# Performance work log

Measured on AMD Instinct MI355X. Metric: run time of the kernel, lower is better.

Reference implementation:

```python
import jax, jax.numpy as jnp
import numpy as np

T = 0.05  # temperature
Z = 8     # number of nearest neighbours


def setup_inputs() -> dict:
    key = jax.random.key(0)
    k1, k2 = jax.random.split(key)
    prototypes = jax.random.normal(k1, (2048, 128), dtype=jnp.float32)
    prototypes = prototypes / jnp.linalg.norm(prototypes, axis=-1, keepdims=True)
    memory_points = jax.random.normal(k2, (131072, 128), dtype=jnp.float32)
    memory_points = memory_points / jnp.linalg.norm(memory_points, axis=-1, keepdims=True)
    return {"prototypes": prototypes, "memory_points": memory_points}


def reference(prototypes, memory_points):
    # [P, N] similarity, exp-scaled (monotonic, kept for faithfulness to the torch code)
    sim = jnp.exp(jnp.einsum('pd,nd->pn', prototypes, memory_points) / T)
    # top-z neighbours per prototype (largest, sorted) -> indices [P, Z]
    _, idx = jax.lax.top_k(sim, Z)
    # gather neighbour points [P, Z, D] and average over the Z neighbours
    pseudo_pro = memory_points[idx].sum(axis=1) / Z  # [P, D]
    # MSELoss with default 'mean' reduction
    loss = jnp.mean((pseudo_pro - prototypes) ** 2)
    return loss
```

## Files before the change

### kernel.cpp

```cpp
#include <hip/hip_runtime.h>
#include <float.h>

#define P 2048
#define N 131072
#define D 128
#define GP 32
#define PBG (P / (GP * 4))
#define NSW 128
#define NPW (N / NSW)
#define NT32 (NPW / 32)
#define CAP 192
#define LCAP 768
#define QS 192.0f
#define VEFF_I 10580
#define VEFF 0.286f

typedef short bf16x8 __attribute__((ext_vector_type(8)));
typedef float f32x4  __attribute__((ext_vector_type(4)));
typedef int   i32x4  __attribute__((ext_vector_type(4)));

union B128 { uint4 u; bf16x8 h; };
union U4I  { uint4 u; i32x4 i; };

__device__ __forceinline__ unsigned int f2bf(float f) {
  unsigned int u = __float_as_uint(f);
  return (u + 0x7FFFu + ((u >> 16) & 1u)) >> 16;
}

__device__ __forceinline__ uint4 pack8(float a0, float a1, float a2, float a3,
                                       float a4, float a5, float a6, float a7) {
  uint4 o;
  o.x = f2bf(a0) | (f2bf(a1) << 16);
  o.y = f2bf(a2) | (f2bf(a3) << 16);
  o.z = f2bf(a4) | (f2bf(a5) << 16);
  o.w = f2bf(a6) | (f2bf(a7) << 16);
  return o;
}

__device__ __forceinline__ unsigned q8(float x) {
  int v = (int)rintf(x * QS);
  v = min(127, max(-127, v));
  return (unsigned)(v & 0xFF);
}

__device__ __forceinline__ unsigned q8x4(const float* r) {
  return q8(r[0]) | (q8(r[1]) << 8) | (q8(r[2]) << 16) | (q8(r[3]) << 24);
}

__device__ __forceinline__ void gld_lds16(const uint4* g, uint4* l) {
  __builtin_amdgcn_global_load_lds((const __attribute__((address_space(1))) void*)g,
                                   (__attribute__((address_space(3))) void*)l, 16, 0, 0);
}

__global__ __launch_bounds__(256) void pack_i8_kernel(
    const float* __restrict__ protos, const float* __restrict__ mem,
    uint4* __restrict__ pPack, uint4* __restrict__ mPack,
    int* __restrict__ cnt, float* __restrict__ out)
{
  __shared__ float lds[32][132];

  const int bi  = blockIdx.x;
  const int tid = threadIdx.x;
  if (bi < 8) { cnt[bi * 256 + tid] = 0; if (bi == 0 && tid == 0) out[0] = 0.0f; }

  const float* src; uint4* dst; int r32;
  if (bi < 64) { src = protos; dst = pPack; r32 = bi; }
  else         { src = mem;    dst = mPack; r32 = bi - 64; }

  #pragma unroll
  for (int i = 0; i < 4; ++i) {
    const int idx = i * 256 + tid;
    const int rr  = idx >> 5;
    const int j   = idx & 31;
    const float4 v = *(const float4*)(src + ((size_t)r32 * 32 + rr) * D + j * 4);
    *(float4*)&lds[rr][j * 4] = v;
  }
  __syncthreads();

  const int h    = tid >> 7;
  const int kt   = (tid >> 6) & 1;
  const int lane = tid & 63;
  const int rowl = h * 16 + (lane & 15);
  const int lw   = lane >> 4;
  const int d0   = kt * 64 + lw * 16;
  const float* r = &lds[rowl][d0];
  uint4 o;
  o.x = q8x4(r);
  o.y = q8x4(r + 4);
  o.z = q8x4(r + 8);
  o.w = q8x4(r + 12);
  dst[(size_t)r32 * 256 + tid] = o;
}

__global__ __launch_bounds__(256, 8) void filter_kernel(
    const uint4* __restrict__ pPack, const uint4* __restrict__ mPack,
    int* __restrict__ cnt, int* __restrict__ cand)
{
  __shared__ uint4 sB[4][256];
  __shared__ unsigned lbuf[LCAP];
  __shared__ int lcnt;

  const int lane = threadIdx.x & 63;
  const int wq   = threadIdx.x >> 6;
  const int b    = blockIdx.x;
  const int xcd  = b & 7;
  const int t8   = b >> 3;
  const int ns   = xcd * (NSW / 8) + (t8 >> 4);
  const int pg   = (t8 & 15) * 4 + wq;
  const int lr   = lane & 15;
  const int lw   = lane >> 4;
  const int prb  = pg * GP + (lw << 2);

  i32x4 A0[2], A1[2];
  #pragma unroll
  for (int kt = 0; kt < 2; ++kt) {
    U4I t0, t1;
    t0.u = pPack[(size_t)((pg * 2 + 0) * 128 + kt * 64) + lane];
    t1.u = pPack[(size_t)((pg * 2 + 1) * 128 + kt * 64) + lane];
    A0[kt] = t0.i;
    A1[kt] = t1.i;
  }

  if (threadIdx.x == 0) lcnt = 0;

#define STAGE(tt, bb)                                                          \
  do {                                                                         \
    const uint4* gsrc = mPack + (size_t)(ns * NT32 + (tt)) * 256;              \
    gld_lds16(gsrc + wq * 64 + lane, &sB[bb][wq * 64]);                        \
  } while (0)

#define APPEND(CV, ROFF)                                                       \
  _Pragma("unroll")                                                            \
  for (int j = 0; j < 4; ++j) {                                                \
    if (CV[j] > VEFF_I) {                                                      \
      const int pr = prb + (ROFF) + j;                                         \
      const int s  = atomicAdd(&lcnt, 1);                                      \
      if (s < LCAP) {                                                          \
        lbuf[s] = ((unsigned)pr << 17) | (unsigned)ptb;                        \
      } else {                                                                 \
        const int gs = atomicAdd(&cnt[pr], 1);                                 \
        if (gs < CAP) cand[(size_t)pr * CAP + gs] = ptb;                       \
      }                                                                        \
    }                                                                          \
  }

#define TILE_BODY(TT)                                                          \
  do {                                                                         \
    const uint4* buf = &sB[(TT) & 3][0];                                       \
    _Pragma("unroll")                                                          \
    for (int h = 0; h < 2; ++h) {                                              \
      U4I b0, b1;                                                              \
      b0.u = buf[h * 128 + 0 * 64 + lane];                                     \
      b1.u = buf[h * 128 + 1 * 64 + lane];                                     \
      i32x4 c0 = {0, 0, 0, 0}, c1 = {0, 0, 0, 0};                              \
      c0 = __builtin_amdgcn_mfma_i32_16x16x64_i8(A0[0], b0.i, c0, 0, 0, 0);    \
      c1 = __builtin_amdgcn_mfma_i32_16x16x64_i8(A1[0], b0.i, c1, 0, 0, 0);    \
      c0 = __builtin_amdgcn_mfma_i32_16x16x64_i8(A0[1], b1.i, c0, 0, 0, 0);    \
      c1 = __builtin_amdgcn_mfma_i32_16x16x64_i8(A1[1], b1.i, c1, 0, 0, 0);    \
      const int cm0 = max(max(c0[0], c0[1]), max(c0[2], c0[3]));               \
      const int cm1 = max(max(c1[0], c1[1]), max(c1[2], c1[3]));               \
      if (max(cm0, cm1) > VEFF_I) {                                            \
        const int ptb = ns * NPW + (TT) * 32 + h * 16 + lr;                    \
        APPEND(c0, 0) APPEND(c1, 16)                                           \
      }                                                                        \
    }                                                                          \
  } while (0)

  STAGE(0, 0);
  STAGE(1, 1);
  #pragma unroll 1
  for (int s = 0; s < NT32 / 2; ++s) {
    if (s + 1 < NT32 / 2) {
      STAGE(2 * s + 2, (2 * s + 2) & 3);
      STAGE(2 * s + 3, (2 * s + 3) & 3);
      asm volatile("s_waitcnt vmcnt(2)" ::: "memory");
    } else {
      asm volatile("s_waitcnt vmcnt(0)" ::: "memory");
    }
    __builtin_amdgcn_s_barrier();
    asm volatile("" ::: "memory");
    __builtin_amdgcn_sched_barrier(0);

    TILE_BODY(2 * s);
    TILE_BODY(2 * s + 1);
  }

  __syncthreads();
  const int n = min(lcnt, LCAP);
  for (int i = threadIdx.x; i < n; i += 256) {
    const unsigned e = lbuf[i];
    const int pr = (int)(e >> 17);
    const int pt = (int)(e & 0x1FFFFu);
    const int s = atomicAdd(&cnt[pr], 1);
    if (s < CAP) cand[(size_t)pr * CAP + s] = pt;
  }
#undef STAGE
#undef APPEND
#undef TILE_BODY
}

__global__ __launch_bounds__(256) void pack_protos_bf16(
    const float* __restrict__ protos, uint4* __restrict__ pPack,
    int* __restrict__ cnt, float* __restrict__ out)
{
  __shared__ float lds[16][132];
  const int bi  = blockIdx.x;
  const int tid = threadIdx.x;
  if (bi < 8) { cnt[bi * 256 + tid] = 0; if (bi == 0 && tid == 0) out[0] = 0.0f; }
  #pragma unroll
  for (int i = 0; i < 2; ++i) {
    const int idx = i * 256 + tid;
    const int rr  = idx >> 5;
    const int j   = idx & 31;
    const float4 v = *(const float4*)(protos + ((size_t)bi * 16 + rr) * D + j * 4);
    *(float4*)&lds[rr][j * 4] = v;
  }
  __syncthreads();
  const int kt = tid >> 6, k8l = (tid >> 4) & 3, rl = tid & 15;
  const int k8 = kt * 4 + k8l;
  const float4 a = *(const float4*)&lds[rl][k8 * 8];
  const float4 b = *(const float4*)&lds[rl][k8 * 8 + 4];
  pPack[(size_t)bi * 256 + tid] = pack8(a.x, a.y, a.z, a.w, b.x, b.y, b.z, b.w);
}

#define NPGF 32
#define NSWF 256
#define NPWF (N / NSWF)
__global__ __launch_bounds__(256, 4) void filter_fallback(
    const uint4* __restrict__ pPack, const float* __restrict__ mem,
    int* __restrict__ cnt, int* __restrict__ cand)
{
  const int lane = threadIdx.x & 63;
  const int b    = blockIdx.x;
  const int xcd  = b & 7;
  const int t8   = b >> 3;
  const int ns   = xcd * (NSWF / 8) + (t8 >> 3);
  const int pg   = (t8 & 7) * 4 + (threadIdx.x >> 6);
  const int lr   = lane & 15;
  const int lw   = lane >> 4;
  const int prb  = pg * 64 + (lw << 2);

  bf16x8 A[4][4];
  #pragma unroll
  for (int pt = 0; pt < 4; ++pt)
    #pragma unroll
    for (int kt = 0; kt < 4; ++kt) {
      B128 tmp; tmp.u = pPack[(size_t)(((pg * 4 + pt) * 4 + kt) * 64) + lane];
      A[pt][kt] = tmp.h;
    }

#define LOADB(BV, NB)                                                          \
  do {                                                                         \
    const float* rp = mem + (size_t)((NB) + lr) * D + lw * 8;                  \
    _Pragma("unroll")                                                          \
    for (int kt = 0; kt < 4; ++kt) {                                           \
      float4 x = *(const float4*)(rp + kt * 32);                               \
      float4 y = *(const float4*)(rp + kt * 32 + 4);                           \
      B128 tmp; tmp.u = pack8(x.x, x.y, x.z, x.w, y.x, y.y, y.z, y.w);         \
      BV[kt] = tmp.h;                                                          \
    }                                                                          \
  } while (0)

#define APPEND(CV, ROFF)                                                       \
  _Pragma("unroll")                                                            \
  for (int j = 0; j < 4; ++j) {                                                \
    if (CV[j] > VEFF) {                                                        \
      const int pr = prb + (ROFF) + j;                                         \
      const int s  = atomicAdd(&cnt[pr], 1);                                   \
      if (s < CAP) cand[(size_t)pr * CAP + s] = ptb;                           \
    }                                                                          \
  }

#define STEP(BV, NB)                                                           \
  do {                                                                         \
    f32x4 c0 = {0.f,0.f,0.f,0.f}, c1 = {0.f,0.f,0.f,0.f};                      \
    f32x4 c2 = {0.f,0.f,0.f,0.f}, c3 = {0.f,0.f,0.f,0.f};                      \
    _Pragma("unroll")                                                          \
    for (int kt = 0; kt < 4; ++kt) {                                           \
      c0 = __builtin_amdgcn_mfma_f32_16x16x32_bf16(A[0][kt], BV[kt], c0, 0, 0, 0); \
      c1 = __builtin_amdgcn_mfma_f32_16x16x32_bf16(A[1][kt], BV[kt], c1, 0, 0, 0); \
      c2 = __builtin_amdgcn_mfma_f32_16x16x32_bf16(A[2][kt], BV[kt], c2, 0, 0, 0); \
      c3 = __builtin_amdgcn_mfma_f32_16x16x32_bf16(A[3][kt], BV[kt], c3, 0, 0, 0); \
    }                                                                          \
    const int ptb = (NB) + lr;                                                 \
    APPEND(c0, 0) APPEND(c1, 16) APPEND(c2, 32) APPEND(c3, 48)                 \
  } while (0)

  const int n0 = ns * NPWF;
  bf16x8 B0[4], B1[4];
  LOADB(B0, n0);
  #pragma unroll 1
  for (int it = 0; it < NPWF / 16; it += 2) {
    const int n = n0 + it * 16;
    LOADB(B1, n + 16);
    STEP(B0, n);
    if (it + 2 < NPWF / 16) LOADB(B0, n + 32);
    STEP(B1, n + 16);
  }
#undef LOADB
#undef APPEND
#undef STEP
}

__global__ __launch_bounds__(512) void merge_kernel(
    const float* __restrict__ protos, const float* __restrict__ mem,
    const int* __restrict__ cnt, const int* __restrict__ cand,
    float* __restrict__ out)
{
  const int p    = blockIdx.x;
  const int tid  = threadIdx.x;
  const int lane = tid & 63;
  const int wid  = tid >> 6;

  __shared__ float cdot[CAP];
  __shared__ int   cidx[CAP];
  __shared__ int   sel[8];

  const int cn = min(cnt[p], CAP);
  const float pr0 = protos[(size_t)p * D + lane];
  const float pr1 = protos[(size_t)p * D + 64 + lane];

  for (int c = wid; c < cn; c += 8) {
    const int idx = cand[(size_t)p * CAP + c];
    const float m0 = mem[(size_t)idx * D + lane];
    const float m1 = mem[(size_t)idx * D + 64 + lane];
    float d = pr0 * m0 + pr1 * m1;
    #pragma unroll
    for (int off = 32; off > 0; off >>= 1) d += __shfl_xor(d, off);
    if (lane == 0) { cdot[c] = d; cidx[c] = idx; }
  }
  __syncthreads();

  if (wid == 0) {
    float v[3]; int vi[3];
    #pragma unroll
    for (int e = 0; e < 3; ++e) {
      const int i = e * 64 + lane;
      if (i < cn) { v[e] = cdot[i]; vi[e] = cidx[i]; }
      else        { v[e] = -FLT_MAX; vi[e] = 0x7FFFFFFF; }
    }
    #pragma unroll 1
    for (int k = 0; k < 8; ++k) {
      float m = -FLT_MAX; int mi = 0x7FFFFFFF;
      #pragma unroll
      for (int e = 0; e < 3; ++e)
        if (v[e] > m || (v[e] == m && vi[e] < mi)) { m = v[e]; mi = vi[e]; }
      #pragma unroll
      for (int off = 32; off > 0; off >>= 1) {
        const float om = __shfl_xor(m, off);
        const int  omi = __shfl_xor(mi, off);
        if (om > m || (om == m && omi < mi)) { m = om; mi = omi; }
      }
      if (lane == 0) sel[k] = (mi == 0x7FFFFFFF) ? 0 : mi;
      #pragma unroll
      for (int e = 0; e < 3; ++e) if (vi[e] == mi) v[e] = -FLT_MAX;
    }
  }
  __syncthreads();

  if (wid == 0) {
    float s0 = 0.f, s1 = 0.f;
    #pragma unroll
    for (int z = 0; z < 8; ++z) {
      const size_t row = (size_t)sel[z] * D;
      s0 += mem[row + lane];
      s1 += mem[row + 64 + lane];
    }
    const float d0 = s0 * 0.125f - pr0;
    const float d1 = s1 * 0.125f - pr1;
    float sq = d0 * d0 + d1 * d1;
    #pragma unroll
    for (int off = 32; off > 0; off >>= 1) sq += __shfl_xor(sq, off);
    if (lane == 0) atomicAdd(out, sq * (1.0f / ((float)P * (float)D)));
  }
}

extern "C" void kernel_launch(void* const* d_in, const int* in_sizes, int n_in,
                              void* d_out, int out_size, void* d_ws, size_t ws_size,
                              hipStream_t stream) {
  const float* protos = (const float*)d_in[0];
  const float* mem    = (const float*)d_in[1];
  float* out = (float*)d_out;

  char* ws = (char*)d_ws;
  int*   cnt   = (int*)ws;
  int*   cand  = (int*)(ws + 8192);
  uint4* pPack = (uint4*)(ws + 8192 + (size_t)P * CAP * 4);
  uint4* mPack = (uint4*)((char*)pPack + (size_t)P * D * 2);

  const size_t need_packed =
      8192 + (size_t)P * CAP * 4 + (size_t)P * D * 2 + (size_t)N * D;

  if (ws_size >= need_packed) {
    pack_i8_kernel<<<dim3(64 + N / 32), 256, 0, stream>>>(
        protos, mem, pPack, mPack, cnt, out);
    filter_kernel<<<dim3(PBG * NSW), 256, 0, stream>>>(pPack, mPack, cnt, cand);
  } else {
    pack_protos_bf16<<<dim3(P / 16), 256, 0, stream>>>(protos, pPack, cnt, out);
    filter_fallback<<<dim3((NPGF * NSWF) / 4), 256, 0, stream>>>(pPack, mem, cnt, cand);
  }
  merge_kernel<<<dim3(P), 512, 0, stream>>>(protos, mem, cnt, cand, out);
}
```

Before: 95.88 us.

## Store int8 candidate scores and prune merge rescoring to a window near 8th best

The filter kernel now stores each candidate's quantized int8 dot product alongside its index. The merge kernel uses these scores to find the approximate 8th-best and rescores in fp32 only candidates within a fixed window of it, cutting gathered memory rows. The filter pipeline also changes from two tiles per iteration with four LDS buffers to one tile per iteration with three buffers, lowering LDS use. The cost is doubled candidate storage and an extra top-8 pass in merge. Exactness depends on the window covering the quantization error.

```diff
diff --git a/kernel.cpp b/kernel.cpp
--- a/kernel.cpp
+++ b/kernel.cpp
@@ -1,5 +1,6 @@
 #include <hip/hip_runtime.h>
 #include <float.h>
+#include <limits.h>
 
 #define P 2048
 #define N 131072
@@ -13,6 +14,7 @@
 #define LCAP 768
 #define QS 192.0f
 #define VEFF_I 10580
+#define WIN 1024
 #define VEFF 0.286f
 
 typedef short bf16x8 __attribute__((ext_vector_type(8)));
@@ -94,10 +96,10 @@
 
 __global__ __launch_bounds__(256, 8) void filter_kernel(
     const uint4* __restrict__ pPack, const uint4* __restrict__ mPack,
-    int* __restrict__ cnt, int* __restrict__ cand)
+    int* __restrict__ cnt, int2* __restrict__ cand)
 {
-  __shared__ uint4 sB[4][256];
-  __shared__ unsigned lbuf[LCAP];
+  __shared__ uint4 sB[3][256];
+  __shared__ int2 lbuf[LCAP];
   __shared__ int lcnt;
 
   const int lane = threadIdx.x & 63;
@@ -136,17 +138,17 @@
       const int pr = prb + (ROFF) + j;                                         \
       const int s  = atomicAdd(&lcnt, 1);                                      \
       if (s < LCAP) {                                                          \
-        lbuf[s] = ((unsigned)pr << 17) | (unsigned)ptb;                        \
+        lbuf[s] = make_int2((pr << 17) | ptb, CV[j]);                          \
       } else {                                                                 \
         const int gs = atomicAdd(&cnt[pr], 1);                                 \
-        if (gs < CAP) cand[(size_t)pr * CAP + gs] = ptb;                       \
+        if (gs < CAP) cand[(size_t)pr * CAP + gs] = make_int2(ptb, CV[j]);     \
       }                                                                        \
     }                                                                          \
   }
 
-#define TILE_BODY(TT)                                                          \
+#define TILE_BODY(TT, BB)                                                      \
   do {                                                                         \
-    const uint4* buf = &sB[(TT) & 3][0];                                       \
+    const uint4* buf = &sB[BB][0];                                             \
     _Pragma("unroll")                                                          \
     for (int h = 0; h < 2; ++h) {                                              \
       U4I b0, b1;                                                              \
@@ -167,13 +169,13 @@
   } while (0)
 
   STAGE(0, 0);
-  STAGE(1, 1);
+  int bc = 0;
   #pragma unroll 1
-  for (int s = 0; s < NT32 / 2; ++s) {
-    if (s + 1 < NT32 / 2) {
-      STAGE(2 * s + 2, (2 * s + 2) & 3);
-      STAGE(2 * s + 3, (2 * s + 3) & 3);
-      asm volatile("s_waitcnt vmcnt(2)" ::: "memory");
+  for (int t = 0; t < NT32; ++t) {
+    const int bn = (bc == 2) ? 0 : bc + 1;
+    if (t + 1 < NT32) {
+      STAGE(t + 1, bn);
+      asm volatile("s_waitcnt vmcnt(1)" ::: "memory");
     } else {
       asm volatile("s_waitcnt vmcnt(0)" ::: "memory");
     }
@@ -181,18 +183,18 @@
     asm volatile("" ::: "memory");
     __builtin_amdgcn_sched_barrier(0);
 
-    TILE_BODY(2 * s);
-    TILE_BODY(2 * s + 1);
+    TILE_BODY(t, bc);
+    bc = bn;
   }
 
   __syncthreads();
   const int n = min(lcnt, LCAP);
   for (int i = threadIdx.x; i < n; i += 256) {
-    const unsigned e = lbuf[i];
-    const int pr = (int)(e >> 17);
-    const int pt = (int)(e & 0x1FFFFu);
+    const int2 e = lbuf[i];
+    const int pr = (int)((unsigned)e.x >> 17);
+    const int pt = e.x & 0x1FFFF;
     const int s = atomicAdd(&cnt[pr], 1);
-    if (s < CAP) cand[(size_t)pr * CAP + s] = pt;
+    if (s < CAP) cand[(size_t)pr * CAP + s] = make_int2(pt, e.y);
   }
 #undef STAGE
 #undef APPEND
@@ -228,7 +230,7 @@
 #define NPWF (N / NSWF)
 __global__ __launch_bounds__(256, 4) void filter_fallback(
     const uint4* __restrict__ pPack, const float* __restrict__ mem,
-    int* __restrict__ cnt, int* __restrict__ cand)
+    int* __restrict__ cnt, int2* __restrict__ cand)
 {
   const int lane = threadIdx.x & 63;
   const int b    = blockIdx.x;
@@ -267,7 +269,8 @@
     if (CV[j] > VEFF) {                                                        \
       const int pr = prb + (ROFF) + j;                                         \
       const int s  = atomicAdd(&cnt[pr], 1);                                   \
-      if (s < CAP) cand[(size_t)pr * CAP + s] = ptb;                           \
+      if (s < CAP) cand[(size_t)pr * CAP + s] =                                \
+          make_int2(ptb, (int)(CV[j] * 36864.0f));                             \
     }                                                                          \
   }
 
@@ -304,7 +307,7 @@
 
 __global__ __launch_bounds__(512) void merge_kernel(
     const float* __restrict__ protos, const float* __restrict__ mem,
-    const int* __restrict__ cnt, const int* __restrict__ cand,
+    const int* __restrict__ cnt, const int2* __restrict__ cand,
     float* __restrict__ out)
 {
   const int p    = blockIdx.x;
@@ -312,16 +315,63 @@
   const int lane = tid & 63;
   const int wid  = tid >> 6;
 
+  __shared__ int   sdot[CAP];
+  __shared__ int   sidx[CAP];
+  __shared__ int   rlist[CAP];
   __shared__ float cdot[CAP];
   __shared__ int   cidx[CAP];
+  __shared__ int   rn, d8s;
   __shared__ int   sel[8];
 
   const int cn = min(cnt[p], CAP);
+  for (int i = tid; i < cn; i += 512) {
+    const int2 e = cand[(size_t)p * CAP + i];
+    sidx[i] = e.x; sdot[i] = e.y;
+  }
+  if (tid == 0) { rn = 0; d8s = INT_MIN; }
+  __syncthreads();
+
+  if (wid == 0 && cn > 8) {
+    int v[3], vi[3];
+    #pragma unroll
+    for (int e = 0; e < 3; ++e) {
+      const int i = e * 64 + lane;
+      if (i < cn) { v[e] = sdot[i]; vi[e] = sidx[i]; }
+      else        { v[e] = INT_MIN; vi[e] = 0x7FFFFFFF; }
+    }
+    int d8 = INT_MIN;
+    #pragma unroll 1
+    for (int k = 0; k < 8; ++k) {
+      int m = INT_MIN, mi = 0x7FFFFFFF;
+      #pragma unroll
+      for (int e = 0; e < 3; ++e)
+        if (v[e] > m || (v[e] == m && vi[e] < mi)) { m = v[e]; mi = vi[e]; }
+      #pragma unroll
+      for (int off = 32; off > 0; off >>= 1) {
+        const int om  = __shfl_xor(m, off);
+        const int omi = __shfl_xor(mi, off);
+        if (om > m || (om == m && omi < mi)) { m = om; mi = omi; }
+      }
+      d8 = m;
+      #pragma unroll
+      for (int e = 0; e < 3; ++e) if (vi[e] == mi) v[e] = INT_MIN;
+    }
+    if (lane == 0) d8s = d8;
+  }
+  __syncthreads();
+
+  const int T = (cn > 8 && d8s > INT_MIN + 2 * WIN) ? (d8s - WIN) : INT_MIN;
+
+  for (int i = tid; i < cn; i += 512) {
+    if (sdot[i] >= T) { const int s = atomicAdd(&rn, 1); rlist[s] = sidx[i]; }
+  }
+  __syncthreads();
+  const int rm = rn;
+
   const float pr0 = protos[(size_t)p * D + lane];
   const float pr1 = protos[(size_t)p * D + 64 + lane];
-
-  for (int c = wid; c < cn; c += 8) {
-    const int idx = cand[(size_t)p * CAP + c];
+  for (int c = wid; c < rm; c += 8) {
+    const int idx = rlist[c];
     const float m0 = mem[(size_t)idx * D + lane];
     const float m1 = mem[(size_t)idx * D + 64 + lane];
     float d = pr0 * m0 + pr1 * m1;
@@ -336,7 +386,7 @@
     #pragma unroll
     for (int e = 0; e < 3; ++e) {
       const int i = e * 64 + lane;
-      if (i < cn) { v[e] = cdot[i]; vi[e] = cidx[i]; }
+      if (i < rm) { v[e] = cdot[i]; vi[e] = cidx[i]; }
       else        { v[e] = -FLT_MAX; vi[e] = 0x7FFFFFFF; }
     }
     #pragma unroll 1
@@ -384,12 +434,12 @@
 
   char* ws = (char*)d_ws;
   int*   cnt   = (int*)ws;
-  int*   cand  = (int*)(ws + 8192);
-  uint4* pPack = (uint4*)(ws + 8192 + (size_t)P * CAP * 4);
+  int2*  cand  = (int2*)(ws + 8192);
+  uint4* pPack = (uint4*)(ws + 8192 + (size_t)P * CAP * 8);
   uint4* mPack = (uint4*)((char*)pPack + (size_t)P * D * 2);
 
   const size_t need_packed =
-      8192 + (size_t)P * CAP * 4 + (size_t)P * D * 2 + (size_t)N * D;
+      8192 + (size_t)P * CAP * 8 + (size_t)P * D * 2 + (size_t)N * D;
 
   if (ws_size >= need_packed) {
     pack_i8_kernel<<<dim3(64 + N / 32), 256, 0, stream>>>(
```

Measured after the change: 100.6 us. +4.9%, slower.
